# Optimization experiments

Hardware: AMD Instinct MI355X
Metric: run time of the kernel (lower is better)

The kernel has to match this reference:

```python
import jax, jax.numpy as jnp
import numpy as np

T, B, C, H, L = 256, 128, 512, 512, 2
WSCALE = 0.03  # keep gates out of hard saturation


def setup_inputs() -> dict:
    key = jax.random.key(0)
    k1, k2, k3 = jax.random.split(key, 3)
    return {
        "input_tensor": jax.random.normal(k1, (T, B, C), jnp.float32),  # (t, b, c), batch_first=False
        "h0": jnp.zeros((L, 4, B, H), jnp.float32),  # per layer: h, c, h_inner, c_inner
        "Wg": jax.random.normal(k2, (L, 4 * H, C + H), jnp.float32) * WSCALE,  # outer Gates
        "bg": jnp.zeros((L, 4 * H), jnp.float32),
        "Wi": jax.random.normal(k3, (L, 4 * H, 2 * H), jnp.float32) * WSCALE,  # inner LSTMCell Gates
        "bi": jnp.zeros((L, 4 * H), jnp.float32),
    }


def _nested_lstm_layer(x, state, Wg, bg, Wi, bi):
    # x: [T, B, C]; state: (h, c, h_inner, c_inner) each [B, H]
    def step(carry, x_t):
        h, c, hi, ci = carry
        # outer cell gates
        g = jnp.concatenate([x_t, h], axis=1) @ Wg.T + bg  # [B, 4H]
        i, f, o, gc = jnp.split(g, 4, axis=1)
        cell = jax.nn.sigmoid(f) * c + jax.nn.sigmoid(i) * jnp.tanh(gc)
        # inner LSTMCell, input = outer candidate cell
        g2 = jnp.concatenate([cell, hi], axis=1) @ Wi.T + bi  # [B, 4H]
        i2, f2, o2, g2c = jnp.split(g2, 4, axis=1)
        ci_n = jax.nn.sigmoid(f2) * ci + jax.nn.sigmoid(i2) * jnp.tanh(g2c)
        hi_n = jax.nn.sigmoid(o2) * jnp.tanh(ci_n)
        # outer cell state is replaced by inner hidden; outer hidden gated on it
        h_n = jax.nn.sigmoid(o) * jnp.tanh(hi_n)
        return (h_n, hi_n, hi_n, ci_n), h_n

    carry, ys = jax.lax.scan(step, state, x)
    return ys, carry  # ys: [T, B, H]


def reference(input_tensor, h0, Wg, bg, Wi, bi):
    x = input_tensor  # already (t, b, c); scan over leading time axis
    n_layers = Wg.shape[0]
    for l in range(n_layers):
        state = (h0[l, 0], h0[l, 1], h0[l, 2], h0[l, 3])
        x, _ = _nested_lstm_layer(x, state, Wg[l], bg[l], Wi[l], bi[l])
    # return_all_layers=False -> last layer output, shape (t, b, h)
    return x
```

## Files before the change

### kernel.cpp

```cpp
#include <hip/hip_runtime.h>

#define T_DIM 256
#define B_DIM 128
#define C_DIM 512
#define H_DIM 512

#define R0H 0
#define PLB 32768

typedef _Float16 half8 __attribute__((ext_vector_type(8)));
typedef float f32x4 __attribute__((ext_vector_type(4)));
typedef unsigned u32x4 __attribute__((ext_vector_type(4)));

__device__ __forceinline__ float sigf(float x) { return 1.0f / (1.0f + __expf(-x)); }
__device__ __forceinline__ float tanhf_(float x) {
  float e = __expf(2.0f * x);
  return (e - 1.0f) / (e + 1.0f);
}

__device__ __forceinline__ half8 cvt8(float4 a, float4 b) {
  half8 h;
  h[0] = (_Float16)a.x; h[1] = (_Float16)a.y; h[2] = (_Float16)a.z; h[3] = (_Float16)a.w;
  h[4] = (_Float16)b.x; h[5] = (_Float16)b.y; h[6] = (_Float16)b.z; h[7] = (_Float16)b.w;
  return h;
}

__device__ __forceinline__ void gbar_arrive(unsigned* slots, int bc, unsigned epoch) {
  __syncthreads();
  if (threadIdx.x == 0) *(volatile unsigned*)(slots + bc) = epoch;
}

__device__ __forceinline__ void gbar_wait_pw(const unsigned* slots, unsigned epoch,
                                             int pollwave) {
  if ((int)(threadIdx.x >> 6) == pollwave) {
    const volatile unsigned* myslot =
        (const volatile unsigned*)(slots + (threadIdx.x & 31));
    int guard = 0;
    for (;;) {
      asm volatile("buffer_inv sc0\n\ts_waitcnt vmcnt(0)" ::: "memory");
      unsigned v = *myslot;
      if (__ballot(v >= epoch) == ~0ull) break;
      if (++guard > (1 << 14)) break;
    }
  }
  __syncthreads();
  asm volatile("buffer_inv sc0" ::: "memory");
  asm volatile("s_waitcnt vmcnt(0)" ::: "memory");
}

__device__ __forceinline__ unsigned sysld_u32(const unsigned* p) {
  unsigned v;
  asm volatile("global_load_dword %0, %1, off sc0 sc1\n\ts_waitcnt vmcnt(0)"
               : "=v"(v) : "v"(p) : "memory");
  return v;
}

__device__ __forceinline__ void xpoll_raw(const unsigned* slots, unsigned epoch) {
  const unsigned* my = slots + (threadIdx.x & 31);
  int guard = 0;
  for (;;) {
    unsigned v = sysld_u32(my);
    if (__ballot(v >= epoch) == ~0ull) break;
    if (++guard > (1 << 15)) break;
  }
}

__device__ __forceinline__ void xpost(unsigned* flag, unsigned epoch) {
  asm volatile("s_waitcnt vmcnt(0)" ::: "memory");
  asm volatile("global_store_dword %0, %1, off sc0 sc1" ::
                   "v"(flag), "v"(epoch) : "memory");
}

__device__ __forceinline__ void store_llc_h16(_Float16* p, _Float16 v) {
  unsigned u = (unsigned)__builtin_bit_cast(unsigned short, v);
  asm volatile("global_store_short %0, %1, off sc0 sc1" ::
                   "v"(p), "v"(u) : "memory");
}

__global__ __launch_bounds__(256, 1) void nlstm_pipe(
    const float* __restrict__ xin, const float* __restrict__ h0,
    const float* __restrict__ Wg, const float* __restrict__ bgb,
    const float* __restrict__ Wi, const float* __restrict__ bib,
    float* __restrict__ out, unsigned* __restrict__ bar,
    _Float16* __restrict__ y0buf, _Float16* __restrict__ hlcb,
    _Float16* __restrict__ hicb, _Float16* __restrict__ clcb)
{
  __shared__ __align__(16) char smem[65536];
  _Float16* AldsH = (_Float16*)smem;
  float* Pl = (float*)(smem + PLB);

  const int tid  = threadIdx.x;
  const int xcd  = blockIdx.x & 7;
  const int lyr  = xcd >> 2;
  const int pgrp = xcd & 3;
  const int bc   = blockIdx.x >> 3;
  const int wv   = tid >> 6;
  const int lane = tid & 63;
  const int ln   = lane & 15;
  const int kg   = lane >> 4;
  const int pb   = tid >> 4;
  const int pj   = tid & 15;
  const int jglob = bc * 16 + pj;
  const int ncol  = bc * 16 + ln;
  const int r0    = pgrp * 32;

  const int exo = (jglob >> 5) * 1024 + (((jglob >> 3) & 3) * 16 + pb) * 8 + (jglob & 7);

  unsigned* eslots = bar + xcd * 64;
  unsigned* cslots = eslots + 32;
  unsigned* fwdS = bar + 512 + pgrp * 32;
  unsigned* bakS = bar + 640 + pgrp * 32;

  _Float16* hloc0 = hlcb + ((size_t)xcd * 2 + 0) * 16384;
  _Float16* hloc1 = hlcb + ((size_t)xcd * 2 + 1) * 16384;
  _Float16* hilc0 = hicb + ((size_t)xcd * 2 + 0) * 16384;
  _Float16* hilc1 = hicb + ((size_t)xcd * 2 + 1) * 16384;
  _Float16* cbase = clcb + (size_t)xcd * 16384;
  _Float16* y0base = y0buf + (size_t)pgrp * 4 * 16384;

  half8 wgf[4][8], wif[4][8];
  float bgv[4], biv[4];
#pragma unroll
  for (int g = 0; g < 4; ++g) {
    const float* wgr = Wg + ((size_t)lyr * 2048 + g * 512 + ncol) * 1024 + wv * 256;
    const float* wir = Wi + ((size_t)lyr * 2048 + g * 512 + ncol) * 1024 + wv * 256;
#pragma unroll
    for (int i = 0; i < 8; ++i) {
      const float* p = wgr + i * 32 + kg * 8;
      wgf[g][i] = cvt8(*(const float4*)p, *(const float4*)(p + 4));
      const float* q = wir + i * 32 + kg * 8;
      wif[g][i] = cvt8(*(const float4*)q, *(const float4*)(q + 4));
    }
    bgv[g] = bgb[lyr * 2048 + g * 512 + jglob];
    biv[g] = bib[lyr * 2048 + g * 512 + jglob];
  }

  float st_c[2], st_ci[2], o_pre[2], outv[2];
  {
    const float* h0l = h0 + (size_t)lyr * 4 * B_DIM * H_DIM + (size_t)(r0 + pb) * H_DIM + jglob;
#pragma unroll
    for (int mt = 0; mt < 2; ++mt) {
      const float* pp = h0l + (size_t)mt * 16 * H_DIM;
      float h_in  = pp[0];
      st_c[mt]    = pp[(size_t)1 * B_DIM * H_DIM];
      float hi_in = pp[(size_t)2 * B_DIM * H_DIM];
      st_ci[mt]   = pp[(size_t)3 * B_DIM * H_DIM];
      hloc0[exo + mt * 512] = (_Float16)h_in;
      hilc0[exo + mt * 512] = (_Float16)hi_in;
      o_pre[mt] = 0.f;
      outv[mt] = 0.f;
    }
  }

  auto stage_x = [&](int t) {
    const int m = tid & 31;
    const int q = tid >> 5;
    const int mt = m >> 4, mm = m & 15;
    const float* srow = xin + ((size_t)t * B_DIM + r0 + m) * C_DIM;
#pragma unroll
    for (int i = 0; i < 8; ++i) {
      const int chunk = q * 8 + i;
      const int ks = chunk >> 2, kq = chunk & 3;
      const float* p = srow + chunk * 8;
      *(half8*)(AldsH + R0H + ks * 1024 + mt * 512 + (kq * 16 + mm) * 8) =
          cvt8(*(const float4*)p, *(const float4*)(p + 4));
    }
  };
  auto copy_r0_sys = [&](const _Float16* src) {
    u32x4 v[8];
#pragma unroll
    for (int i = 0; i < 8; ++i) {
      const u32x4* p = (const u32x4*)(src + (i * 256 + tid) * 8);
      asm volatile("global_load_dwordx4 %0, %1, off sc0 sc1"
                   : "=v"(v[i]) : "v"(p) : "memory");
    }
    asm volatile("s_waitcnt vmcnt(0)" ::: "memory");
    __builtin_amdgcn_sched_barrier(0);
#pragma unroll
    for (int i = 0; i < 8; ++i)
      *(u32x4*)(AldsH + R0H + (i * 256 + tid) * 8) = v[i];
  };
  auto mfma8 = [&](const _Float16* rb, int ksb, half8 (&wf)[4][8], f32x4 (&acc)[2][4]) {
#pragma unroll
    for (int i = 0; i < 8; ++i) {
      const _Float16* ab = rb + (ksb + i) * 1024 + lane * 8;
      half8 a0 = *(const half8*)(ab);
      half8 a1 = *(const half8*)(ab + 512);
#pragma unroll
      for (int g = 0; g < 4; ++g) {
        acc[0][g] = __builtin_amdgcn_mfma_f32_16x16x32_f16(a0, wf[g][i], acc[0][g], 0, 0, 0);
        acc[1][g] = __builtin_amdgcn_mfma_f32_16x16x32_f16(a1, wf[g][i], acc[1][g], 0, 0, 0);
      }
    }
  };
  auto plw = [&](f32x4 (&acc)[2][4]) {
#pragma unroll
    for (int mt = 0; mt < 2; ++mt)
#pragma unroll
      for (int g = 0; g < 4; ++g)
#pragma unroll
        for (int rr = 0; rr < 4; ++rr)
          Pl[(((g * 2 + mt) * 16 + kg * 4 + rr) * 16 + ln) * 4 + (wv ^ kg)] = acc[mt][g][rr];
  };
  auto plsum = [&](int g, int mt) -> float {
    f32x4 v = *(const f32x4*)(Pl + (((g * 2 + mt) * 16 + pb) * 16 + pj) * 4);
    return v[0] + v[1] + v[2] + v[3];
  };

  unsigned eseq = 0, cseq = 0;

  gbar_arrive(eslots, bc, ++eseq);
  if (lyr == 0) stage_x(0);
  gbar_wait_pw(eslots, eseq, 3);
  if (lyr == 1) {
    if (wv == 0) xpoll_raw(fwdS, 1u);
    __syncthreads();
    copy_r0_sys(y0base + 0);
    __syncthreads();
    if (tid == 0) xpost(bakS + bc, 1u);
  }
  if (wv < 2) {
    f32x4 acc[2][4];
#pragma unroll
    for (int mt = 0; mt < 2; ++mt)
#pragma unroll
      for (int g = 0; g < 4; ++g) acc[mt][g] = (f32x4){0.f, 0.f, 0.f, 0.f};
    mfma8(AldsH + R0H, 8 * wv, wgf, acc);
    plw(acc);
  }

  for (int t = 0; t < T_DIM; ++t) {
    const int pr = t & 1;
    _Float16* hrd  = pr ? hloc1 : hloc0;
    _Float16* hwr  = pr ? hloc0 : hloc1;
    _Float16* hird = pr ? hilc1 : hilc0;
    _Float16* hiwr = pr ? hilc0 : hilc1;
    _Float16* y0wr = y0base + (size_t)(t & 3) * 16384;
    _Float16* y0rd = y0base + (size_t)((t + 1) & 3) * 16384;

    if (wv >= 2) {
      f32x4 acc[2][4];
#pragma unroll
      for (int mt = 0; mt < 2; ++mt)
#pragma unroll
        for (int g = 0; g < 4; ++g) acc[mt][g] = (f32x4){0.f, 0.f, 0.f, 0.f};
      mfma8(hrd, 8 * wv - 16, wgf, acc);
      plw(acc);
    }
    __syncthreads();

#pragma unroll
    for (int mt = 0; mt < 2; ++mt) {
      float gi = plsum(0, mt) + bgv[0];
      float gf = plsum(1, mt) + bgv[1];
      float go = plsum(2, mt) + bgv[2];
      float gc = plsum(3, mt) + bgv[3];
      float cell = sigf(gf) * st_c[mt] + sigf(gi) * tanhf_(gc);
      o_pre[mt] = go;
      cbase[exo + mt * 512] = (_Float16)cell;
    }
    gbar_arrive(cslots, bc, ++cseq);
    if (wv >= 2) {
      f32x4 acc[2][4];
#pragma unroll
      for (int mt = 0; mt < 2; ++mt)
#pragma unroll
        for (int g = 0; g < 4; ++g) acc[mt][g] = (f32x4){0.f, 0.f, 0.f, 0.f};
      mfma8(hird, 8 * wv - 16, wif, acc);
      plw(acc);
    }
    gbar_wait_pw(cslots, cseq, 0);

    if (wv < 2) {
      f32x4 acc[2][4];
#pragma unroll
      for (int mt = 0; mt < 2; ++mt)
#pragma unroll
        for (int g = 0; g < 4; ++g) acc[mt][g] = (f32x4){0.f, 0.f, 0.f, 0.f};
      mfma8(cbase, 8 * wv, wif, acc);
      plw(acc);
    }
    __syncthreads();

#pragma unroll
    for (int mt = 0; mt < 2; ++mt) {
      float i2 = plsum(0, mt) + biv[0];
      float f2 = plsum(1, mt) + biv[1];
      float o2 = plsum(2, mt) + biv[2];
      float c2 = plsum(3, mt) + biv[3];
      float ci_n = sigf(f2) * st_ci[mt] + sigf(i2) * tanhf_(c2);
      float hi_n = sigf(o2) * tanhf_(ci_n);
      float h_n  = sigf(o_pre[mt]) * tanhf_(hi_n);
      st_ci[mt] = ci_n;
      st_c[mt]  = hi_n;
      hiwr[exo + mt * 512] = (_Float16)hi_n;
      hwr[exo + mt * 512]  = (_Float16)h_n;
      if (lyr == 0) {
        store_llc_h16(y0wr + exo + mt * 512, (_Float16)h_n);
      } else {
        outv[mt] = h_n;
      }
    }

    gbar_arrive(eslots, bc, ++eseq);
    if (lyr == 0) {
      if (tid == 0) xpost(fwdS + bc, (unsigned)(t + 1));
      if (t + 1 < T_DIM) {
        stage_x(t + 1);
        __syncthreads();
        if (wv < 2) {
          f32x4 acc[2][4];
#pragma unroll
          for (int mt = 0; mt < 2; ++mt)
#pragma unroll
            for (int g = 0; g < 4; ++g) acc[mt][g] = (f32x4){0.f, 0.f, 0.f, 0.f};
          mfma8(AldsH + R0H, 8 * wv, wgf, acc);
          plw(acc);
        } else if (wv == 3 && t >= 2) {
          xpoll_raw(bakS, (unsigned)(t - 2));
        }
      }
    } else {
#pragma unroll
      for (int mt = 0; mt < 2; ++mt)
        out[((size_t)t * B_DIM + (r0 + pb + mt * 16)) * H_DIM + jglob] = outv[mt];
      if (t + 1 < T_DIM) {
        if (wv == 0) xpoll_raw(fwdS, (unsigned)(t + 2));
        __syncthreads();
        copy_r0_sys(y0rd);
        __syncthreads();
        if (tid == 0) xpost(bakS + bc, (unsigned)(t + 2));
        if (wv < 2) {
          f32x4 acc[2][4];
#pragma unroll
          for (int mt = 0; mt < 2; ++mt)
#pragma unroll
            for (int g = 0; g < 4; ++g) acc[mt][g] = (f32x4){0.f, 0.f, 0.f, 0.f};
          mfma8(AldsH + R0H, 8 * wv, wgf, acc);
          plw(acc);
        }
      }
    }
    gbar_wait_pw(eslots, eseq, 3);
  }
}

extern "C" void kernel_launch(void* const* d_in, const int* in_sizes, int n_in,
                              void* d_out, int out_size, void* d_ws, size_t ws_size,
                              hipStream_t stream) {
  const float* xin = (const float*)d_in[0];
  const float* h0  = (const float*)d_in[1];
  const float* Wg  = (const float*)d_in[2];
  const float* bg  = (const float*)d_in[3];
  const float* Wi  = (const float*)d_in[4];
  const float* bi  = (const float*)d_in[5];
  float* out = (float*)d_out;

  unsigned* bar  = (unsigned*)d_ws;
  _Float16* y0b  = (_Float16*)((char*)d_ws + 4096);
  _Float16* hlcb = y0b + (size_t)4 * 4 * 16384;
  _Float16* hicb = hlcb + (size_t)8 * 2 * 16384;
  _Float16* clcb = hicb + (size_t)8 * 2 * 16384;

  hipMemsetAsync(d_ws, 0, 4096, stream);

  nlstm_pipe<<<dim3(256), dim3(256), 0, stream>>>(
      xin, h0, Wg, bg, Wi, bi, out, bar, y0b, hlcb, hicb, clcb);
}
```

Baseline: 2.592 ms.

## Stage next-step inputs by idle waves and copy recurrent operands into LDS

Waves 0-1 now prefetch the next timestep's x (layer 0) or y0 (layer 1) while waves 2-3 run the h-recurrent MFMA, which removes the separate staging phase and its extra block barriers after the elementwise step. The h, h_inner and cell operands are copied from global buffers into dedicated LDS regions before the MFMA loops instead of being read directly. This doubles shared memory to 128KB. It adds per-step copy work on the critical recurrent path, and the layer-1 back-post now occurs earlier.

```diff
diff --git a/kernel.cpp b/kernel.cpp
--- a/kernel.cpp
+++ b/kernel.cpp
@@ -5,8 +5,10 @@
 #define C_DIM 512
 #define H_DIM 512
 
-#define R0H 0
-#define PLB 32768
+#define RxH 0
+#define RhcH 16384
+#define RhiH 32768
+#define PLB 98304
 
 typedef _Float16 half8 __attribute__((ext_vector_type(8)));
 typedef float f32x4 __attribute__((ext_vector_type(4)));
@@ -85,7 +87,7 @@
     _Float16* __restrict__ y0buf, _Float16* __restrict__ hlcb,
     _Float16* __restrict__ hicb, _Float16* __restrict__ clcb)
 {
-  __shared__ __align__(16) char smem[65536];
+  __shared__ __align__(16) char smem[131072];
   _Float16* AldsH = (_Float16*)smem;
   float* Pl = (float*)(smem + PLB);
 
@@ -152,33 +154,78 @@
     }
   }
 
-  auto stage_x = [&](int t) {
-    const int m = tid & 31;
-    const int q = tid >> 5;
-    const int mt = m >> 4, mm = m & 15;
-    const float* srow = xin + ((size_t)t * B_DIM + r0 + m) * C_DIM;
+  auto stage_x_ws = [&](int t) {
+    const float* sb = xin + ((size_t)t * B_DIM + r0) * C_DIM;
 #pragma unroll
     for (int i = 0; i < 8; ++i) {
-      const int chunk = q * 8 + i;
-      const int ks = chunk >> 2, kq = chunk & 3;
-      const float* p = srow + chunk * 8;
-      *(half8*)(AldsH + R0H + ks * 1024 + mt * 512 + (kq * 16 + mm) * 8) =
-          cvt8(*(const float4*)p, *(const float4*)(p + 4));
-    }
-  };
-  auto copy_r0_sys = [&](const _Float16* src) {
-    u32x4 v[8];
-#pragma unroll
-    for (int i = 0; i < 8; ++i) {
-      const u32x4* p = (const u32x4*)(src + (i * 256 + tid) * 8);
-      asm volatile("global_load_dwordx4 %0, %1, off sc0 sc1"
-                   : "=v"(v[i]) : "v"(p) : "memory");
-    }
-    asm volatile("s_waitcnt vmcnt(0)" ::: "memory");
-    __builtin_amdgcn_sched_barrier(0);
-#pragma unroll
-    for (int i = 0; i < 8; ++i)
-      *(u32x4*)(AldsH + R0H + (i * 256 + tid) * 8) = v[i];
+      const int ks = 8 * wv + i;
+#pragma unroll
+      for (int rep = 0; rep < 2; ++rep) {
+        const int combo = rep * 64 + lane;
+        const int kq = combo >> 5;
+        const int mrow = combo & 31;
+        const int mt = mrow >> 4, mm = mrow & 15;
+        const float* p = sb + (size_t)mrow * C_DIM + ks * 32 + kq * 8;
+        *(half8*)(AldsH + RxH + ks * 1024 + mt * 512 + (kq * 16 + mm) * 8) =
+            cvt8(*(const float4*)p, *(const float4*)(p + 4));
+      }
+    }
+  };
+  auto copy_y0_ws = [&](const _Float16* src) {
+#pragma unroll
+    for (int b = 0; b < 2; ++b) {
+      u32x4 v[8];
+#pragma unroll
+      for (int i = 0; i < 8; ++i) {
+        const int idx = wv * 1024 + b * 512 + i * 64 + lane;
+        const u32x4* p = (const u32x4*)(src + idx * 8);
+        asm volatile("global_load_dwordx4 %0, %1, off sc0 sc1"
+                     : "=v"(v[i]) : "v"(p) : "memory");
+      }
+      asm volatile("s_waitcnt vmcnt(0)" ::: "memory");
+      __builtin_amdgcn_sched_barrier(0);
+#pragma unroll
+      for (int i = 0; i < 8; ++i) {
+        const int idx = wv * 1024 + b * 512 + i * 64 + lane;
+        *(u32x4*)(AldsH + RxH + idx * 8) = v[i];
+      }
+    }
+  };
+  auto copy_hhi_w23 = [&](const _Float16* hrd, const _Float16* hird) {
+    const int ub = (wv - 2) * 1024;
+#pragma unroll
+    for (int b = 0; b < 2; ++b) {
+      u32x4 v[8];
+#pragma unroll
+      for (int i = 0; i < 8; ++i)
+        v[i] = *(const u32x4*)(hrd + (ub + b * 512 + i * 64 + lane) * 8);
+#pragma unroll
+      for (int i = 0; i < 8; ++i)
+        *(u32x4*)(AldsH + RhcH + (ub + b * 512 + i * 64 + lane) * 8) = v[i];
+    }
+#pragma unroll
+    for (int b = 0; b < 2; ++b) {
+      u32x4 v[8];
+#pragma unroll
+      for (int i = 0; i < 8; ++i)
+        v[i] = *(const u32x4*)(hird + (ub + b * 512 + i * 64 + lane) * 8);
+#pragma unroll
+      for (int i = 0; i < 8; ++i)
+        *(u32x4*)(AldsH + RhiH + (ub + b * 512 + i * 64 + lane) * 8) = v[i];
+    }
+  };
+  auto copy_rc_ws = [&]() {
+    const int ub = wv * 1024;
+#pragma unroll
+    for (int b = 0; b < 2; ++b) {
+      u32x4 v[8];
+#pragma unroll
+      for (int i = 0; i < 8; ++i)
+        v[i] = *(const u32x4*)(cbase + (ub + b * 512 + i * 64 + lane) * 8);
+#pragma unroll
+      for (int i = 0; i < 8; ++i)
+        *(u32x4*)(AldsH + RhcH + (ub + b * 512 + i * 64 + lane) * 8) = v[i];
+    }
   };
   auto mfma8 = [&](const _Float16* rb, int ksb, half8 (&wf)[4][8], f32x4 (&acc)[2][4]) {
 #pragma unroll
@@ -210,12 +257,13 @@
   unsigned eseq = 0, cseq = 0;
 
   gbar_arrive(eslots, bc, ++eseq);
-  if (lyr == 0) stage_x(0);
+  if (lyr == 0 && wv < 2) stage_x_ws(0);
   gbar_wait_pw(eslots, eseq, 3);
   if (lyr == 1) {
-    if (wv == 0) xpoll_raw(fwdS, 1u);
-    __syncthreads();
-    copy_r0_sys(y0base + 0);
+    if (wv < 2) {
+      xpoll_raw(fwdS, 1u);
+      copy_y0_ws(y0base + 0);
+    }
     __syncthreads();
     if (tid == 0) xpost(bakS + bc, 1u);
   }
@@ -225,7 +273,7 @@
     for (int mt = 0; mt < 2; ++mt)
 #pragma unroll
       for (int g = 0; g < 4; ++g) acc[mt][g] = (f32x4){0.f, 0.f, 0.f, 0.f};
-    mfma8(AldsH + R0H, 8 * wv, wgf, acc);
+    mfma8(AldsH + RxH, 8 * wv, wgf, acc);
     plw(acc);
   }
 
@@ -239,15 +287,25 @@
     _Float16* y0rd = y0base + (size_t)((t + 1) & 3) * 16384;
 
     if (wv >= 2) {
+      copy_hhi_w23(hrd, hird);
       f32x4 acc[2][4];
 #pragma unroll
       for (int mt = 0; mt < 2; ++mt)
 #pragma unroll
         for (int g = 0; g < 4; ++g) acc[mt][g] = (f32x4){0.f, 0.f, 0.f, 0.f};
-      mfma8(hrd, 8 * wv - 16, wgf, acc);
+      mfma8(AldsH + RhcH, 8 * wv - 16, wgf, acc);
       plw(acc);
+    } else if (t + 1 < T_DIM) {
+      if (lyr == 0) {
+        stage_x_ws(t + 1);
+      } else {
+        xpoll_raw(fwdS, (unsigned)(t + 2));
+        copy_y0_ws(y0rd);
+      }
     }
     __syncthreads();
+    if (lyr == 1 && tid == 0 && t + 1 < T_DIM)
+      xpost(bakS + bc, (unsigned)(t + 2));
 
 #pragma unroll
     for (int mt = 0; mt < 2; ++mt) {
@@ -266,18 +324,19 @@
       for (int mt = 0; mt < 2; ++mt)
 #pragma unroll
         for (int g = 0; g < 4; ++g) acc[mt][g] = (f32x4){0.f, 0.f, 0.f, 0.f};
-      mfma8(hird, 8 * wv - 16, wif, acc);
+      mfma8(AldsH + RhiH, 8 * wv - 16, wif, acc);
       plw(acc);
     }
     gbar_wait_pw(cslots, cseq, 0);
 
     if (wv < 2) {
+      copy_rc_ws();
       f32x4 acc[2][4];
 #pragma unroll
       for (int mt = 0; mt < 2; ++mt)
 #pragma unroll
         for (int g = 0; g < 4; ++g) acc[mt][g] = (f32x4){0.f, 0.f, 0.f, 0.f};
-      mfma8(cbase, 8 * wv, wif, acc);
+      mfma8(AldsH + RhcH, 8 * wv, wif, acc);
       plw(acc);
     }
     __syncthreads();
@@ -306,15 +365,13 @@
     if (lyr == 0) {
       if (tid == 0) xpost(fwdS + bc, (unsigned)(t + 1));
       if (t + 1 < T_DIM) {
-        stage_x(t + 1);
-        __syncthreads();
         if (wv < 2) {
           f32x4 acc[2][4];
 #pragma unroll
           for (int mt = 0; mt < 2; ++mt)
 #pragma unroll
             for (int g = 0; g < 4; ++g) acc[mt][g] = (f32x4){0.f, 0.f, 0.f, 0.f};
-          mfma8(AldsH + R0H, 8 * wv, wgf, acc);
+          mfma8(AldsH + RxH, 8 * wv, wgf, acc);
           plw(acc);
         } else if (wv == 3 && t >= 2) {
           xpoll_raw(bakS, (unsigned)(t - 2));
@@ -324,21 +381,14 @@
 #pragma unroll
       for (int mt = 0; mt < 2; ++mt)
         out[((size_t)t * B_DIM + (r0 + pb + mt * 16)) * H_DIM + jglob] = outv[mt];
-      if (t + 1 < T_DIM) {
-        if (wv == 0) xpoll_raw(fwdS, (unsigned)(t + 2));
-        __syncthreads();
-        copy_r0_sys(y0rd);
-        __syncthreads();
-        if (tid == 0) xpost(bakS + bc, (unsigned)(t + 2));
-        if (wv < 2) {
-          f32x4 acc[2][4];
-#pragma unroll
-          for (int mt = 0; mt < 2; ++mt)
-#pragma unroll
-            for (int g = 0; g < 4; ++g) acc[mt][g] = (f32x4){0.f, 0.f, 0.f, 0.f};
-          mfma8(AldsH + R0H, 8 * wv, wgf, acc);
-          plw(acc);
-        }
+      if (t + 1 < T_DIM && wv < 2) {
+        f32x4 acc[2][4];
+#pragma unroll
+        for (int mt = 0; mt < 2; ++mt)
+#pragma unroll
+          for (int g = 0; g < 4; ++g) acc[mt][g] = (f32x4){0.f, 0.f, 0.f, 0.f};
+        mfma8(AldsH + RxH, 8 * wv, wgf, acc);
+        plw(acc);
       }
     }
     gbar_wait_pw(eslots, eseq, 3);
```

Result: slower. 2.918 ms (+12.6%).
